# Performance work log

Measured on AMD Instinct MI355X. Metric: run time of the kernel, lower is better.

Reference implementation:

```python
import jax, jax.numpy as jnp
import numpy as np

N = 65536      # num ref nodes
M = 65536      # num query nodes
E = 1572864    # num edges (avg degree 24)
K0 = 27        # num kernels (3x3x3 neighborhood)
D1 = 64        # input channels
D2 = 64        # output channels


def setup_inputs() -> dict:
    key = jax.random.key(0)
    k1, k2, k3, k4, k5, k6 = jax.random.split(key, 6)
    # kernel init mirrors initialize_kernel_weight (uniform in [-bound, bound])
    fan_in = D1 * K0
    gain = float(np.sqrt(2.0 / (1.0 + 5.0)))  # leaky_relu gain with slope sqrt(5)
    std = gain / np.sqrt(fan_in)
    bound = float(np.sqrt(3.0) * std)
    kernel = jax.random.uniform(k1, (K0, D1, D2), minval=-bound, maxval=bound, dtype=jnp.float32)
    ref_feat = jax.random.normal(k2, (N, D1), dtype=jnp.float32)
    e_kernel = jax.random.randint(k3, (E,), 0, K0)
    e_ref = jax.random.randint(k4, (E,), 0, N)
    e_query = jax.random.randint(k5, (E,), 0, M)
    e_weight = jax.random.uniform(k6, (E,), dtype=jnp.float32)
    return {
        "kernel": kernel,
        "ref_feat": ref_feat,
        "e_kernel": e_kernel,
        "e_ref": e_ref,
        "e_query": e_query,
        "num_queries": M,
        "e_weight": e_weight,
    }


def reference(kernel, ref_feat, e_kernel, e_ref, e_query, num_queries, e_weight):
    # Math of MessagePassing.forward:
    #   query_feat[m] = sum_{edges e: e_query[e]==m} w_e * (ref_feat[e_ref[e]] @ kernel[e_kernel[e]])
    # Efficient form: precompute each node's transform under every kernel
    # (N*K0*D1*D2 dense GEMM), then gather per edge and scatter-reduce.
    transformed = jnp.einsum('nd,kdo->nko', ref_feat, kernel)   # [N, K0, D2]
    msgs = transformed[e_ref, e_kernel] * e_weight[:, None]      # [E, D2]
    query_feat = jax.ops.segment_sum(msgs, e_query, num_segments=num_queries)  # [M, D2]
    return query_feat
```

## Files before the change

### kernel.cpp

```cpp
#include <hip/hip_runtime.h>

#define DIN 64
#define DOUT 64
#define MAXK 32

typedef __bf16 bf16x8 __attribute__((ext_vector_type(8)));
typedef float  f32x4  __attribute__((ext_vector_type(4)));

static __device__ inline unsigned short f2b(float x) {
    return __builtin_bit_cast(unsigned short, (__bf16)x);
}
static __device__ inline float b2f(unsigned short u) {
    return __uint_as_float(((unsigned int)u) << 16);
}


__global__ void conv_w_kernel(const float* __restrict__ W,
                              unsigned short* __restrict__ Wt, int total) {
    int i = blockIdx.x * blockDim.x + threadIdx.x;
    if (i < total) {
        int j    = i & 7;
        int lane = (i >> 3) & 63;
        int h    = (i >> 9) & 1;
        int t    = (i >> 10) & 3;
        int k    = i >> 12;
        int col  = lane & 15;
        int quad = lane >> 4;
        int d1 = h * 32 + quad * 8 + j;
        int d2 = t * 16 + col;
        Wt[i] = f2b(W[(k * 64 + d1) * 64 + d2]);
    }
}


__global__ __launch_bounds__(256) void phaseA_kernel(
    const float* __restrict__ ref,
    const unsigned short* __restrict__ Wt,
    unsigned short* __restrict__ T,
    int K0, int Nn)
{
    const int lane = threadIdx.x & 63;
    const int wid  = threadIdx.x >> 6;
    const int col  = lane & 15;
    const int quad = lane >> 4;
    const int n0   = blockIdx.x * 64 + wid * 16;
    const int row  = n0 + col;

    __shared__ __align__(16) char ldsbuf[4][16 * 144];
    char* buf = ldsbuf[wid];

    const float* rp = ref + (size_t)row * 64;
    f32x4 r0 = *reinterpret_cast<const f32x4*>(rp + quad * 8);
    f32x4 r1 = *reinterpret_cast<const f32x4*>(rp + quad * 8 + 4);
    f32x4 r2 = *reinterpret_cast<const f32x4*>(rp + 32 + quad * 8);
    f32x4 r3 = *reinterpret_cast<const f32x4*>(rp + 32 + quad * 8 + 4);
    bf16x8 b0, b1;
    #pragma unroll
    for (int i = 0; i < 4; ++i) {
        b0[i]     = (__bf16)r0[i];
        b0[4 + i] = (__bf16)r1[i];
        b1[i]     = (__bf16)r2[i];
        b1[4 + i] = (__bf16)r3[i];
    }

    const int rrow = lane >> 2;
    const int rq   = lane & 3;

    for (int k = 0; k < K0; ++k) {
        const unsigned short* Wk = Wt + (size_t)k * 4096;
        #pragma unroll
        for (int t = 0; t < 4; ++t) {
            const unsigned short* ap = Wk + (size_t)t * 1024 + lane * 8;
            bf16x8 a0 = *reinterpret_cast<const bf16x8*>(ap);
            bf16x8 a1 = *reinterpret_cast<const bf16x8*>(ap + 512);
            f32x4 c = {0.f, 0.f, 0.f, 0.f};
            c = __builtin_amdgcn_mfma_f32_16x16x32_bf16(a0, b0, c, 0, 0, 0);
            c = __builtin_amdgcn_mfma_f32_16x16x32_bf16(a1, b1, c, 0, 0, 0);
            unsigned int lo = (unsigned int)f2b(c[0]) | ((unsigned int)f2b(c[1]) << 16);
            unsigned int hi = (unsigned int)f2b(c[2]) | ((unsigned int)f2b(c[3]) << 16);
            *reinterpret_cast<uint2*>(buf + col * 144 + t * 32 + quad * 8) =
                make_uint2(lo, hi);
        }
        uint4 v0 = *reinterpret_cast<const uint4*>(buf + rrow * 144 + rq * 32);
        uint4 v1 = *reinterpret_cast<const uint4*>(buf + rrow * 144 + rq * 32 + 16);
        size_t gbase = ((size_t)k * Nn + n0 + rrow) * 64 + rq * 16;
        *reinterpret_cast<uint4*>(T + gbase)     = v0;
        *reinterpret_cast<uint4*>(T + gbase + 8) = v1;
    }
}


__global__ void p1_hist_kernel(const int* __restrict__ eq, int E,
                               int* __restrict__ qcount) {
    __shared__ int l[256];
    l[threadIdx.x] = 0;
    __syncthreads();
    int stride = gridDim.x * blockDim.x;
    for (int i = blockIdx.x * blockDim.x + threadIdx.x; i < E; i += stride)
        atomicAdd(&l[((unsigned)eq[i]) >> 8], 1);
    __syncthreads();
    int v = l[threadIdx.x];
    if (v) atomicAdd(&qcount[threadIdx.x], v);
}

__global__ void p1_scan_kernel(const int* __restrict__ qcount,
                               int* __restrict__ gbase, int* __restrict__ gcursor,
                               int* __restrict__ qstart, int NB, int M, int E) {
    __shared__ int sh[256];
    int t = threadIdx.x;
    int v = (t < NB) ? qcount[t] : 0;
    sh[t] = v;
    __syncthreads();
    #pragma unroll
    for (int o = 1; o < 256; o <<= 1) {
        int x = (t >= o) ? sh[t - o] : 0;
        __syncthreads();
        sh[t] += x;
        __syncthreads();
    }
    int ex = sh[t] - v;
    if (t < NB) { gbase[t] = ex; gcursor[t] = ex; }
    if (t == 0) qstart[M] = E;
}

__global__ __launch_bounds__(256) void p1_scatter_kernel(
    const int* __restrict__ eq, const int* __restrict__ er,
    const int* __restrict__ ek, const float* __restrict__ ew,
    int E, int* __restrict__ gcursor, uint2* __restrict__ tmp)
{
    __shared__ int bin[256];
    __shared__ int base[256];
    const int t = threadIdx.x;
    bin[t] = 0;
    __syncthreads();
    const int i0 = blockIdx.x * 4096;
    unsigned key[16];
    unsigned rank[16];
    uint2 pay[16];
    #pragma unroll
    for (int u = 0; u < 16; ++u) {
        int i = i0 + u * 256 + t;
        if (i < E) {
            int q = eq[i];
            unsigned b = ((unsigned)q) >> 8;
            key[u] = b;
            rank[u] = atomicAdd(&bin[b], 1);
            pay[u] = make_uint2((unsigned)er[i] | ((unsigned)ek[i] << 16) |
                                ((unsigned)(q & 255) << 21),
                                __float_as_uint(ew[i]));
        } else {
            key[u] = 0xFFFFFFFFu;
        }
    }
    __syncthreads();
    int c = bin[t];
    if (c) base[t] = atomicAdd(&gcursor[t], c);
    __syncthreads();
    #pragma unroll
    for (int u = 0; u < 16; ++u) {
        if (key[u] != 0xFFFFFFFFu)
            tmp[(size_t)base[key[u]] + rank[u]] = pay[u];
    }
}

__global__ __launch_bounds__(256) void p2_kernel(
    const uint2* __restrict__ tmp, const int* __restrict__ gbase,
    const int* __restrict__ qcount, uint2* __restrict__ rec,
    int* __restrict__ qstart)
{
    __shared__ int fine[256];
    __shared__ int foff[256];
    const int b = blockIdx.x;
    const int t = threadIdx.x;
    const int s = gbase[b];
    const int L = qcount[b];
    fine[t] = 0;
    __syncthreads();
    for (int i = t; i < L; i += 256)
        atomicAdd(&fine[(tmp[s + i].x >> 21) & 255], 1);
    __syncthreads();
    int v = fine[t];
    __syncthreads();
    #pragma unroll
    for (int o = 1; o < 256; o <<= 1) {
        int x = (t >= o) ? fine[t - o] : 0;
        __syncthreads();
        fine[t] += x;
        __syncthreads();
    }
    foff[t] = fine[t] - v;
    qstart[b * 256 + t] = s + foff[t];
    __syncthreads();
    fine[t] = 0;
    __syncthreads();
    for (int i = t; i < L; i += 256) {
        uint2 p = tmp[s + i];
        unsigned fb = (p.x >> 21) & 255;
        int r = atomicAdd(&fine[fb], 1);
        rec[(size_t)s + foff[fb] + r] = p;
    }
}


__global__ __launch_bounds__(256) void phaseB_kernel(
    const unsigned short* __restrict__ T,
    const uint2* __restrict__ rec,
    const int* __restrict__ qstart,
    float* __restrict__ out, int Nn)
{
    const int lane = threadIdx.x & 63;
    const int wid  = threadIdx.x >> 6;
    const int q    = blockIdx.x * 4 + wid;

    int beg = qstart[q];
    int end = qstart[q + 1];
    int cnt = end - beg;
    float acc = 0.f;

    if (cnt <= 64) {
        uint2 rv = make_uint2(0u, 0u);
        if (lane < cnt) rv = rec[beg + lane];
        int j = 0;
        for (; j + 8 <= cnt; j += 8) {
            float partial[8];
            #pragma unroll
            for (int u = 0; u < 8; ++u) {
                unsigned mx = (unsigned)__shfl((int)rv.x, j + u);
                unsigned mw = (unsigned)__shfl((int)rv.y, j + u);
                unsigned short tv =
                    T[((size_t)((mx >> 16) & 31) * Nn + (mx & 0xFFFFu)) * 64 + lane];
                partial[u] = __uint_as_float(mw) * b2f(tv);
            }
            #pragma unroll
            for (int u = 0; u < 8; ++u) acc += partial[u];
        }
        for (; j < cnt; ++j) {
            unsigned mx = (unsigned)__shfl((int)rv.x, j);
            unsigned mw = (unsigned)__shfl((int)rv.y, j);
            acc = fmaf(__uint_as_float(mw),
                       b2f(T[((size_t)((mx >> 16) & 31) * Nn + (mx & 0xFFFFu)) * 64 + lane]),
                       acc);
        }
    } else {
        for (int j = beg; j < end; ++j) {
            uint2 v0 = rec[j];
            unsigned m0 = __builtin_amdgcn_readfirstlane(v0.x);
            float w0 = __uint_as_float(__builtin_amdgcn_readfirstlane(v0.y));
            acc = fmaf(w0,
                       b2f(T[((size_t)((m0 >> 16) & 31) * Nn + (m0 & 0xFFFFu)) * 64 + lane]),
                       acc);
        }
    }
    out[(size_t)q * 64 + lane] = acc;
}


__global__ void hist_kernel(const int* __restrict__ ek, int E, int* __restrict__ counts) {
    __shared__ int l[MAXK];
    if (threadIdx.x < MAXK) l[threadIdx.x] = 0;
    __syncthreads();
    int stride = gridDim.x * blockDim.x;
    for (int i = blockIdx.x * blockDim.x + threadIdx.x; i < E; i += stride)
        atomicAdd(&l[ek[i]], 1);
    __syncthreads();
    if (threadIdx.x < MAXK) {
        int v = l[threadIdx.x];
        if (v) atomicAdd(&counts[threadIdx.x], v);
    }
}

__global__ void scan_kernel(const int* __restrict__ counts, int K,
                            int* __restrict__ start, int* __restrict__ cursor) {
    if (threadIdx.x == 0 && blockIdx.x == 0) {
        int acc = 0;
        for (int k = 0; k < K; ++k) {
            start[k] = acc;
            cursor[k] = acc;
            acc += counts[k];
        }
    }
}

__global__ void scatter_kernel(const int* __restrict__ ek, int E,
                               int* __restrict__ cursor, int* __restrict__ sorted) {
    __shared__ int lcnt[MAXK], lbase[MAXK], lpos[MAXK];
    if (threadIdx.x < MAXK) { lcnt[threadIdx.x] = 0; lpos[threadIdx.x] = 0; }
    __syncthreads();
    int i = blockIdx.x * blockDim.x + threadIdx.x;
    int k = 0;
    bool valid = (i < E);
    if (valid) { k = ek[i]; atomicAdd(&lcnt[k], 1); }
    __syncthreads();
    if (threadIdx.x < MAXK) {
        int v = lcnt[threadIdx.x];
        if (v) lbase[threadIdx.x] = atomicAdd(&cursor[threadIdx.x], v);
    }
    __syncthreads();
    if (valid) {
        int slot = lbase[k] + atomicAdd(&lpos[k], 1);
        sorted[slot] = i;
    }
}

__global__ __launch_bounds__(256) void mp_bucket_kernel(
    const float* __restrict__ W, const float* __restrict__ ref,
    const int* __restrict__ e_ref, const int* __restrict__ e_query,
    const float* __restrict__ e_weight, const int* __restrict__ sorted,
    const int* __restrict__ start, const int* __restrict__ counts,
    float* __restrict__ out)
{
    const int k = blockIdx.y;
    const int lane = threadIdx.x & 63;
    const int wid = threadIdx.x >> 6;

    float wreg[DIN];
    const float* Wk = W + k * DIN * DOUT;
    #pragma unroll
    for (int d = 0; d < DIN; ++d) wreg[d] = Wk[d * DOUT + lane];

    const int s = start[k];
    const int c = counts[k];
    const int nwaves = gridDim.x * 4;

    for (int i = blockIdx.x * 4 + wid; i < c; i += nwaves) {
        int eid = __builtin_amdgcn_readfirstlane(sorted[s + i]);
        int r = e_ref[eid];
        int q = e_query[eid];
        float w = e_weight[eid];
        const float* row = ref + r * DIN;
        float a0 = 0.f, a1 = 0.f, a2 = 0.f, a3 = 0.f;
        #pragma unroll
        for (int d = 0; d < DIN; d += 4) {
            a0 += row[d + 0] * wreg[d + 0];
            a1 += row[d + 1] * wreg[d + 1];
            a2 += row[d + 2] * wreg[d + 2];
            a3 += row[d + 3] * wreg[d + 3];
        }
        atomicAdd(&out[q * DOUT + lane], ((a0 + a1) + (a2 + a3)) * w);
    }
}


extern "C" void kernel_launch(void* const* d_in, const int* in_sizes, int n_in,
                              void* d_out, int out_size, void* d_ws, size_t ws_size,
                              hipStream_t stream) {
    const float* W        = (const float*)d_in[0];
    const float* ref      = (const float*)d_in[1];
    const int*   e_kernel = (const int*)d_in[2];
    const int*   e_ref    = (const int*)d_in[3];
    const int*   e_query  = (const int*)d_in[4];
    const float* e_weight = (const float*)d_in[6];

    const int K0 = in_sizes[0] / (DIN * DOUT);
    const int N  = in_sizes[1] / DIN;
    const int E  = in_sizes[2];
    const int M  = out_size / DOUT;
    const int KD = K0 * 64;
    const int NB = M / 256;

    float* out = (float*)d_out;

    size_t off = 0;
    auto alloc = [&](size_t bytes, size_t align) {
        off = (off + align - 1) / align * align;
        size_t r = off; off += bytes; return r;
    };
    size_t o_tmp     = alloc((size_t)E * 8, 16);
    size_t o_rec     = alloc((size_t)E * 8, 16);
    size_t o_qstart  = alloc((size_t)(M + 1) * 4, 4);
    size_t o_qcount  = alloc(256 * 4, 4);
    size_t o_gbase   = alloc(256 * 4, 4);
    size_t o_gcursor = alloc(256 * 4, 4);
    size_t o_wt      = alloc((size_t)K0 * 4096 * 2, 16);
    size_t o_T       = alloc((size_t)N * KD * 2, 16);
    size_t needA = off;

    bool planA_ok = (ws_size >= needA) && (M % 256 == 0) && (NB >= 1) && (NB <= 256) &&
                    (N % 64 == 0) && (N <= 65536) && (K0 <= 32);

    if (planA_ok) {
        char* ws = (char*)d_ws;
        uint2* tmp           = (uint2*)(ws + o_tmp);
        uint2* rec           = (uint2*)(ws + o_rec);
        int*  qstart         = (int*)(ws + o_qstart);
        int*  qcount         = (int*)(ws + o_qcount);
        int*  gbase          = (int*)(ws + o_gbase);
        int*  gcursor        = (int*)(ws + o_gcursor);
        unsigned short* Wt   = (unsigned short*)(ws + o_wt);
        unsigned short* T    = (unsigned short*)(ws + o_T);

        conv_w_kernel<<<(K0 * 4096 + 255) / 256, 256, 0, stream>>>(W, Wt, K0 * 4096);

        hipMemsetAsync(qcount, 0, 256 * 4, stream);
        p1_hist_kernel<<<512, 256, 0, stream>>>(e_query, E, qcount);
        p1_scan_kernel<<<1, 256, 0, stream>>>(qcount, gbase, gcursor, qstart, NB, M, E);
        p1_scatter_kernel<<<(E + 4095) / 4096, 256, 0, stream>>>(e_query, e_ref, e_kernel,
                                                                 e_weight, E, gcursor, tmp);
        p2_kernel<<<NB, 256, 0, stream>>>(tmp, gbase, qcount, rec, qstart);

        phaseA_kernel<<<N / 64, 256, 0, stream>>>(ref, Wt, T, K0, N);

        phaseB_kernel<<<M / 4, 256, 0, stream>>>(T, rec, qstart, out, N);
    } else {
        hipMemsetAsync(out, 0, (size_t)out_size * sizeof(float), stream);
        size_t needB = (size_t)(96 + E) * sizeof(int);
        if (ws_size >= needB) {
            int* ws_i   = (int*)d_ws;
            int* counts = ws_i;
            int* start  = ws_i + 32;
            int* cursor = ws_i + 64;
            int* sorted = ws_i + 96;
            hipMemsetAsync(counts, 0, 96 * sizeof(int), stream);
            hist_kernel<<<512, 256, 0, stream>>>(e_kernel, E, counts);
            scan_kernel<<<1, 64, 0, stream>>>(counts, K0, start, cursor);
            scatter_kernel<<<(E + 255) / 256, 256, 0, stream>>>(e_kernel, E, cursor, sorted);
            dim3 grid(64, K0);
            mp_bucket_kernel<<<grid, 256, 0, stream>>>(W, ref, e_ref, e_query, e_weight,
                                                       sorted, start, counts, out);
        }
    }
}
```

Baseline: 282.6 us.

## Double-buffer edge gathers in phaseB and use nontemporal T stores/loads

The per-query gather loop in phaseB now processes edges in padded groups of 8 and ping-pongs two register buffers. It issues the next group's T loads before accumulating the current group, so more memory requests are in flight. Padded lanes use zero weights, which keeps the result correct and removes the scalar tail loop. T is written and gathered with nontemporal hints to reduce cache pollution from the large transformed table. The risks are higher register use, which can lower occupancy, and losing whatever L2 reuse the gathers had.

```diff
diff --git a/kernel.cpp b/kernel.cpp
--- a/kernel.cpp
+++ b/kernel.cpp
@@ -6,6 +6,7 @@
 
 typedef __bf16 bf16x8 __attribute__((ext_vector_type(8)));
 typedef float  f32x4  __attribute__((ext_vector_type(4)));
+typedef unsigned int u32x4 __attribute__((ext_vector_type(4)));
 
 static __device__ inline unsigned short f2b(float x) {
     return __builtin_bit_cast(unsigned short, (__bf16)x);
@@ -81,11 +82,11 @@
             *reinterpret_cast<uint2*>(buf + col * 144 + t * 32 + quad * 8) =
                 make_uint2(lo, hi);
         }
-        uint4 v0 = *reinterpret_cast<const uint4*>(buf + rrow * 144 + rq * 32);
-        uint4 v1 = *reinterpret_cast<const uint4*>(buf + rrow * 144 + rq * 32 + 16);
+        u32x4 v0 = *reinterpret_cast<const u32x4*>(buf + rrow * 144 + rq * 32);
+        u32x4 v1 = *reinterpret_cast<const u32x4*>(buf + rrow * 144 + rq * 32 + 16);
         size_t gbase = ((size_t)k * Nn + n0 + rrow) * 64 + rq * 16;
-        *reinterpret_cast<uint4*>(T + gbase)     = v0;
-        *reinterpret_cast<uint4*>(T + gbase + 8) = v1;
+        __builtin_nontemporal_store(v0, reinterpret_cast<u32x4*>(T + gbase));
+        __builtin_nontemporal_store(v1, reinterpret_cast<u32x4*>(T + gbase + 8));
     }
 }
 
@@ -202,6 +203,24 @@
 }
 
 
+#define PB_ISSUE(TB, WB, BASE)                                                  \
+    {                                                                           \
+        _Pragma("unroll")                                                       \
+        for (int u = 0; u < 8; ++u) {                                           \
+            unsigned mx = (unsigned)__shfl((int)rv.x, (BASE) + u);              \
+            unsigned mw = (unsigned)__shfl((int)rv.y, (BASE) + u);              \
+            TB[u] = __builtin_nontemporal_load(                                 \
+                T + ((size_t)((mx >> 16) & 31) * Nn + (mx & 0xFFFFu)) * 64 + lane); \
+            WB[u] = __uint_as_float(mw);                                        \
+        }                                                                       \
+    }
+
+#define PB_CONSUME(TB, WB)                                                      \
+    {                                                                           \
+        _Pragma("unroll")                                                       \
+        for (int u = 0; u < 8; ++u) acc = fmaf(WB[u], b2f(TB[u]), acc);         \
+    }
+
 __global__ __launch_bounds__(256) void phaseB_kernel(
     const unsigned short* __restrict__ T,
     const uint2* __restrict__ rec,
@@ -217,31 +236,23 @@
     int cnt = end - beg;
     float acc = 0.f;
 
-    if (cnt <= 64) {
+    if (cnt > 0 && cnt <= 64) {
         uint2 rv = make_uint2(0u, 0u);
         if (lane < cnt) rv = rec[beg + lane];
-        int j = 0;
-        for (; j + 8 <= cnt; j += 8) {
-            float partial[8];
-            #pragma unroll
-            for (int u = 0; u < 8; ++u) {
-                unsigned mx = (unsigned)__shfl((int)rv.x, j + u);
-                unsigned mw = (unsigned)__shfl((int)rv.y, j + u);
-                unsigned short tv =
-                    T[((size_t)((mx >> 16) & 31) * Nn + (mx & 0xFFFFu)) * 64 + lane];
-                partial[u] = __uint_as_float(mw) * b2f(tv);
-            }
-            #pragma unroll
-            for (int u = 0; u < 8; ++u) acc += partial[u];
-        }
-        for (; j < cnt; ++j) {
-            unsigned mx = (unsigned)__shfl((int)rv.x, j);
-            unsigned mw = (unsigned)__shfl((int)rv.y, j);
-            acc = fmaf(__uint_as_float(mw),
-                       b2f(T[((size_t)((mx >> 16) & 31) * Nn + (mx & 0xFFFFu)) * 64 + lane]),
-                       acc);
-        }
-    } else {
+        const int ng = (cnt + 7) >> 3;
+
+        unsigned short tA[8], tB[8];
+        float wA[8], wB[8];
+
+        PB_ISSUE(tA, wA, 0)
+        for (int g = 0; g < ng; g += 2) {
+            if (g + 1 < ng) PB_ISSUE(tB, wB, (g + 1) * 8)
+            PB_CONSUME(tA, wA)
+            if (g + 1 >= ng) break;
+            if (g + 2 < ng) PB_ISSUE(tA, wA, (g + 2) * 8)
+            PB_CONSUME(tB, wB)
+        }
+    } else if (cnt > 64) {
         for (int j = beg; j < end; ++j) {
             uint2 v0 = rec[j];
             unsigned m0 = __builtin_amdgcn_readfirstlane(v0.x);
```

Result: slower. 326.0 us (+15.3%).
